# Kernel tuning notes

Measured on AMD Instinct MI355X. Metric: run time of the kernel, lower is better.

The kernel has to match this reference:

```python
import jax, jax.numpy as jnp
import numpy as np

B, S, D = 8, 1024, 1024
H = 16
DK = D // H  # 64, dim_k == dim_v
F = 4096
EPS = 1e-5


def _layernorm(x, w, b):
    mu = jnp.mean(x, axis=-1, keepdims=True)
    var = jnp.mean((x - mu) ** 2, axis=-1, keepdims=True)
    return (x - mu) * jax.lax.rsqrt(var + EPS) * w + b


def setup_inputs() -> dict:
    key = jax.random.key(0)
    ks = jax.random.split(key, 12)
    init = lambda k, shape: (jax.random.normal(k, shape, dtype=jnp.float32) * 0.02)
    return {
        "src": jax.random.normal(ks[0], (B, S, D), dtype=jnp.float32),
        "mask": jnp.zeros((S, S), dtype=jnp.float32),
        # per-head projections, stacked over heads: [H, D, DK]
        "Wq": init(ks[1], (H, D, DK)), "bq": jnp.zeros((H, DK), jnp.float32),
        "Wk": init(ks[2], (H, D, DK)), "bk": jnp.zeros((H, DK), jnp.float32),
        "Wv": init(ks[3], (H, D, DK)), "bv": jnp.zeros((H, DK), jnp.float32),
        "Wo": init(ks[4], (H * DK, D)), "bo": jnp.zeros((D,), jnp.float32),
        "ln1_w": jnp.ones((D,), jnp.float32), "ln1_b": jnp.zeros((D,), jnp.float32),
        "W1": init(ks[5], (D, F)), "b1": jnp.zeros((F,), jnp.float32),
        "W2": init(ks[6], (F, D)), "b2": jnp.zeros((D,), jnp.float32),
        "ln2_w": jnp.ones((D,), jnp.float32), "ln2_b": jnp.zeros((D,), jnp.float32),
    }


def reference(src, mask, Wq, bq, Wk, bk, Wv, bv, Wo, bo,
              ln1_w, ln1_b, W1, b1, W2, b2, ln2_w, ln2_b):
    # per-head projections (vectorized over heads): [B, H, S, DK]
    q = jnp.einsum('bsd,hdk->bhsk', src, Wq) + bq[None, :, None, :]
    k = jnp.einsum('bsd,hdk->bhsk', src, Wk) + bk[None, :, None, :]
    v = jnp.einsum('bsd,hdk->bhsk', src, Wv) + bv[None, :, None, :]
    scale = float(DK) ** 0.5
    logits = jnp.einsum('bhsk,bhtk->bhst', q, k) / scale  # [B,H,S,S]
    logits = logits + mask * (-1e9)
    attn = jax.nn.softmax(logits, axis=-1)
    ctx = jnp.einsum('bhst,bhtv->bhsv', attn, v)  # [B,H,S,DK]
    # concat heads along feature dim (head-major order matches torch cat)
    ctx = jnp.transpose(ctx, (0, 2, 1, 3)).reshape(B, S, H * DK)
    attn_out = ctx @ Wo + bo
    x = _layernorm(src + attn_out, ln1_w, ln1_b)
    ffn = jax.nn.relu(x @ W1 + b1) @ W2 + b2
    return _layernorm(x + ffn, ln2_w, ln2_b)
```

## Files before the change

kernel.cpp:

```cpp
#include <hip/hip_runtime.h>

#define BB 8
#define SS 1024
#define DD 1024
#define HH 16
#define DK 64
#define FF 4096
#define MM (BB*SS)

typedef __attribute__((ext_vector_type(8))) short short8;
typedef __attribute__((ext_vector_type(4))) short short4v;
typedef __attribute__((ext_vector_type(4))) float floatx4;

__device__ inline short f2bf(float f) {
  union { float f; unsigned u; } v; v.f = f;
  unsigned r = (v.u + 0x7FFFu + ((v.u >> 16) & 1u)) >> 16;
  return (short)r;
}
__device__ inline float bf2f(unsigned short u) {
  union { unsigned u; float f; } v; v.u = ((unsigned)u) << 16;
  return v.f;
}

__device__ inline void gload_lds16(const void* g, void* l) {
  __builtin_amdgcn_global_load_lds(
      (const __attribute__((address_space(1))) void*)g,
      (__attribute__((address_space(3))) void*)l, 16, 0, 0);
}

__device__ void tr64(const float* __restrict__ s, unsigned short* __restrict__ d,
                     int R, int C, int r0, int c0, float (*ld)[68], int tid) {
  {
    int r = tid >> 2, c16 = (tid & 3) * 16;
#pragma unroll
    for (int i = 0; i < 4; ++i)
      *(float4*)(&ld[r][c16 + i * 4]) =
          *(const float4*)(s + (size_t)(r0 + r) * C + c0 + c16 + i * 4);
  }
  __syncthreads();
  int c = tid >> 2, r16 = (tid & 3) * 16;
  short8 o0, o1;
#pragma unroll
  for (int i = 0; i < 8; ++i) {
    o0[i] = f2bf(ld[r16 + i][c]);
    o1[i] = f2bf(ld[r16 + 8 + i][c]);
  }
  unsigned short* dp = d + (size_t)(c0 + c) * R + r0 + r16;
  *(short8*)(dp) = o0;
  *(short8*)(dp + 8) = o1;
}

__global__ __launch_bounds__(256) void prep_all(
    const float* __restrict__ src,
    const float* __restrict__ Wq, const float* __restrict__ Wk,
    const float* __restrict__ Wv,
    const float* __restrict__ bq, const float* __restrict__ bk,
    const float* __restrict__ bv, const float* __restrict__ Wo,
    unsigned short* __restrict__ srcb, unsigned short* __restrict__ wqkvT,
    float* __restrict__ bqkv, unsigned short* __restrict__ woT) {
  __shared__ float ld[64][68];
  const int bid = blockIdx.x, tid = threadIdx.x;
  if (bid < 4096) {
    int i8 = (bid * 256 + tid) * 8;
    float4 a = *(const float4*)(src + i8);
    float4 b = *(const float4*)(src + i8 + 4);
    short8 o;
    o[0] = f2bf(a.x); o[1] = f2bf(a.y); o[2] = f2bf(a.z); o[3] = f2bf(a.w);
    o[4] = f2bf(b.x); o[5] = f2bf(b.y); o[6] = f2bf(b.z); o[7] = f2bf(b.w);
    *(short8*)(srcb + i8) = o;
  } else if (bid < 4864) {
    int idx = bid - 4096;
    int d0 = (idx & 15) * 64, h = (idx >> 4) & 15, z = idx >> 8;
    const float* W = (z == 0 ? Wq : z == 1 ? Wk : Wv) + (size_t)h * DD * DK;
    {
      int r = tid >> 2, c16 = (tid & 3) * 16;
#pragma unroll
      for (int i = 0; i < 4; ++i)
        *(float4*)(&ld[r][c16 + i * 4]) =
            *(const float4*)(W + (size_t)(d0 + r) * DK + c16 + i * 4);
    }
    __syncthreads();
    int dv = tid >> 2, d16 = (tid & 3) * 16;
    short8 o0, o1;
#pragma unroll
    for (int i = 0; i < 8; ++i) {
      o0[i] = f2bf(ld[d16 + i][dv]);
      o1[i] = f2bf(ld[d16 + 8 + i][dv]);
    }
    unsigned short* dst = wqkvT + (size_t)(z * 1024 + h * 64 + dv) * DD + d0 + d16;
    *(short8*)(dst) = o0;
    *(short8*)(dst + 8) = o1;
  } else if (bid < 4876) {
    int n = (bid - 4864) * 256 + tid;
    int z = n >> 10;
    const float* s = (z == 0 ? bq : z == 1 ? bk : bv);
    bqkv[n] = s[n & 1023];
  } else {
    int idx = bid - 4876;
    tr64(Wo, woT, 1024, 1024, (idx & 15) * 64, (idx >> 4) * 64, ld, tid);
  }
}

__global__ __launch_bounds__(256) void prep2(
    const unsigned short* __restrict__ qkv, const float* __restrict__ mask,
    const float* __restrict__ W1, const float* __restrict__ W2,
    unsigned short* __restrict__ kbb, unsigned short* __restrict__ vtb,
    unsigned short* __restrict__ maskb, unsigned short* __restrict__ w1T,
    unsigned short* __restrict__ w2T) {
  __shared__ float ldf[64][68];
  const int bid = blockIdx.x, tid = threadIdx.x;
  if (bid < 2048) {
    const int t0 = (bid & 15) * 64, h = (bid >> 4) & 15, b = bid >> 8;
    int row = tid >> 2, c = (tid & 3) * 16;
    const unsigned short* s = qkv + (size_t)(b * SS + t0 + row) * 3072 + 1024 + h * 64 + c;
    unsigned short* d = kbb + ((size_t)((b * HH + h) * SS + t0 + row)) * 64 + c;
    *(short8*)(d) = *(const short8*)(s);
    *(short8*)(d + 8) = *(const short8*)(s + 8);
  } else if (bid < 4096) {
    __shared__ unsigned short ld[64][72];
    const int i = bid - 2048;
    const int t0 = (i & 15) * 64, h = (i >> 4) & 15, b = i >> 8;
    {
      int r = tid >> 2, c16 = (tid & 3) * 16;
      const unsigned short* s = qkv + (size_t)(b * SS + t0 + r) * 3072 + 2048 + h * 64 + c16;
      *(short8*)(&ld[r][c16]) = *(const short8*)(s);
      *(short8*)(&ld[r][c16 + 8]) = *(const short8*)(s + 8);
    }
    __syncthreads();
    int dv = tid >> 2, t16 = (tid & 3) * 16;
    short8 o0, o1;
#pragma unroll
    for (int j = 0; j < 8; ++j) {
      o0[j] = (short)ld[t16 + j][dv];
      o1[j] = (short)ld[t16 + 8 + j][dv];
    }
    unsigned short* d = vtb + ((size_t)(b * HH + h) * DK + dv) * SS + t0 + t16;
    *(short8*)(d) = o0;
    *(short8*)(d + 8) = o1;
  } else if (bid < 4608) {
    int i8 = ((bid - 4096) * 256 + tid) * 8;
    float4 a = *(const float4*)(mask + i8);
    float4 b = *(const float4*)(mask + i8 + 4);
    short8 o;
    o[0] = f2bf(a.x * -1e9f); o[1] = f2bf(a.y * -1e9f);
    o[2] = f2bf(a.z * -1e9f); o[3] = f2bf(a.w * -1e9f);
    o[4] = f2bf(b.x * -1e9f); o[5] = f2bf(b.y * -1e9f);
    o[6] = f2bf(b.z * -1e9f); o[7] = f2bf(b.w * -1e9f);
    *(short8*)(maskb + i8) = o;
  } else if (bid < 5632) {
    int i = bid - 4608;
    tr64(W1, w1T, 1024, 4096, (i & 15) * 64, (i >> 4) * 64, ldf, tid);
  } else {
    int i = bid - 5632;
    tr64(W2, w2T, 4096, 1024, (i & 63) * 64, (i >> 6) * 64, ldf, tid);
  }
}

#define BARE __builtin_amdgcn_s_barrier()
#define VM6  asm volatile("s_waitcnt vmcnt(6)" ::: "memory")
#define VM4  asm volatile("s_waitcnt vmcnt(4)" ::: "memory")
#define VM0  asm volatile("s_waitcnt vmcnt(0)" ::: "memory")
#define PH_HINT asm volatile("s_waitcnt lgkmcnt(8)" ::: "memory")
#define PH_SYNC { \
  __builtin_amdgcn_s_barrier(); \
  asm volatile("s_waitcnt lgkmcnt(0)" ::: "memory"); \
  __builtin_amdgcn_sched_barrier(0); }

#define LOAD_A(lA_, mh_) { \
  _Pragma("unroll") for (int m_ = 0; m_ < 4; ++m_) { \
    const int row_ = wr * 128 + (mh_) * 64 + m_ * 16 + lm; \
    _Pragma("unroll") for (int ks_ = 0; ks_ < 2; ++ks_) \
      a[m_][ks_] = *(const short8*)((lA_) + (size_t)row_ * 64 + \
                     (size_t)(((ks_ * 4 + quad) ^ (lm & 7)) * 8)); \
  } }

#define LOAD_B(lB_, nh_) { \
  _Pragma("unroll") for (int n_ = 0; n_ < 2; ++n_) { \
    const int row_ = wc * 64 + (nh_) * 32 + n_ * 16 + lm; \
    _Pragma("unroll") for (int ks_ = 0; ks_ < 2; ++ks_) \
      bfr[nh_][n_][ks_] = *(const short8*)((lB_) + 16384 + (size_t)row_ * 64 + \
                     (size_t)(((ks_ * 4 + quad) ^ (lm & 7)) * 8)); \
  } }

#define STAGE_A(kt_, mh_, lb_) { \
  _Pragma("unroll") for (int c_ = 0; c_ < 2; ++c_) { \
    const int row_ = c_ * 128 + (mh_) * 64; \
    gload_lds16(gA + (size_t)(kt_) * 64 + (size_t)row_ * K, \
                (lb_) + (size_t)(row_ + wave * 8) * 64); \
  } }

#define STAGE_B(kt_, nh_, lb_) { \
  _Pragma("unroll") for (int c_ = 0; c_ < 2; ++c_) { \
    const int row_ = c_ * 128 + hi128 + (nh_) * 32; \
    gload_lds16(gB + (size_t)(kt_) * 64 + (size_t)row_ * K, \
                (lb_) + 16384 + (size_t)(row_ + (wave & 3) * 8) * 64); \
  } }

#define MFMA_PH(mh_, nh_) { \
  __builtin_amdgcn_s_setprio(1); \
  _Pragma("unroll") for (int m_ = 0; m_ < 4; ++m_) \
    _Pragma("unroll") for (int n_ = 0; n_ < 2; ++n_) { \
      acc[(mh_) * 4 + m_][(nh_) * 2 + n_] = __builtin_amdgcn_mfma_f32_16x16x32_bf16( \
          bfr[nh_][n_][0], a[m_][0], acc[(mh_) * 4 + m_][(nh_) * 2 + n_], 0, 0, 0); \
      acc[(mh_) * 4 + m_][(nh_) * 2 + n_] = __builtin_amdgcn_mfma_f32_16x16x32_bf16( \
          bfr[nh_][n_][1], a[m_][1], acc[(mh_) * 4 + m_][(nh_) * 2 + n_], 0, 0, 0); \
    } \
  __builtin_amdgcn_s_setprio(0); }

#define KITER(e_, ST_) { \
  LOAD_A(buf0, 0); LOAD_B(buf0, 0); \
  STAGE_B((e_) + 1, 1, buf1); \
  PH_HINT; PH_SYNC; MFMA_PH(0, 0); BARE; \
  LOAD_B(buf0, 1); \
  if (ST_) STAGE_A((e_) + 2, 0, buf0); \
  PH_SYNC; MFMA_PH(0, 1); BARE; \
  LOAD_A(buf0, 1); \
  if (ST_) STAGE_B((e_) + 2, 0, buf0); \
  PH_SYNC; MFMA_PH(1, 0); BARE; \
  if (ST_) STAGE_A((e_) + 2, 1, buf0); \
  PH_SYNC; MFMA_PH(1, 1); \
  if (ST_) { VM6; } else { VM0; } \
  BARE; \
  LOAD_A(buf1, 0); LOAD_B(buf1, 0); \
  if (ST_) STAGE_B((e_) + 2, 1, buf0); \
  PH_HINT; PH_SYNC; MFMA_PH(0, 0); BARE; \
  LOAD_B(buf1, 1); \
  if (ST_) STAGE_A((e_) + 3, 0, buf1); \
  PH_SYNC; MFMA_PH(0, 1); BARE; \
  LOAD_A(buf1, 1); \
  if (ST_) STAGE_B((e_) + 3, 0, buf1); \
  PH_SYNC; MFMA_PH(1, 0); BARE; \
  if (ST_) { \
    STAGE_A((e_) + 3, 1, buf1); \
    PH_SYNC; MFMA_PH(1, 1); VM6; BARE; \
  } else { \
    PH_SYNC; MFMA_PH(1, 1); \
  } }

template <int RELU>
__global__ __launch_bounds__(512, 2) void gemm256(
    const unsigned short* __restrict__ A, const unsigned short* __restrict__ Bt,
    const float* __restrict__ bias, unsigned short* __restrict__ C,
    int M, int N, int K) {
  extern __shared__ unsigned short lds[];
  unsigned short* buf0 = lds;
  unsigned short* buf1 = lds + 32768;
  const int tid = threadIdx.x;
  const int wave = tid >> 6, lane = tid & 63;
  const int lm = lane & 15, quad = lane >> 4;
  const int wr = wave >> 2, wc = wave & 3;

  const int nwg = gridDim.x;
  const int cpx = nwg >> 3;
  const int id = (blockIdx.x & 7) * cpx + (blockIdx.x >> 3);
  const int nbx = N >> 8;
  const int bx = id % nbx, by = id / nbx;
  const int n0 = bx << 8, m0 = by << 8;

  const int NT = K >> 6;

  const int srow = tid >> 3;
  const int chs = (tid & 7) ^ (srow & 7);
  const int hi128 = (tid >= 256) ? 64 : 0;
  const int r32 = (tid >> 3) & 31;
  const unsigned short* gA = A + (size_t)(m0 + srow) * K + chs * 8;
  const unsigned short* gB = Bt + (size_t)(n0 + r32) * K + chs * 8;

  floatx4 acc[8][4] = {};
  short8 a[4][2], bfr[2][2][2];

  STAGE_A(0, 0, buf0); STAGE_B(0, 0, buf0);
  STAGE_A(0, 1, buf0); STAGE_B(0, 1, buf0);
  STAGE_A(1, 0, buf1); STAGE_B(1, 0, buf1);
  STAGE_A(1, 1, buf1);
  VM6;
  BARE;

  const int TT = NT >> 1;
  for (int i = 0; i < TT - 1; ++i) {
    KITER(2 * i, 1);
  }
  KITER(NT - 2, 0);

#pragma unroll
  for (int mi = 0; mi < 8; ++mi) {
    const int row = m0 + wr * 128 + mi * 16 + lm;
#pragma unroll
    for (int nj = 0; nj < 4; ++nj) {
      const int col = n0 + wc * 64 + nj * 16 + (quad << 2);
      const float4 bv = *(const float4*)(bias + col);
      float vv[4] = {acc[mi][nj][0] + bv.x, acc[mi][nj][1] + bv.y,
                     acc[mi][nj][2] + bv.z, acc[mi][nj][3] + bv.w};
      short4v o;
#pragma unroll
      for (int r = 0; r < 4; ++r) {
        float v = vv[r];
        if (RELU) v = fmaxf(v, 0.f);
        o[r] = f2bf(v);
      }
      *(short4v*)(C + (size_t)row * N + col) = o;
    }
  }
}

#define LOAD_A1(lb_, mh_) { \
  _Pragma("unroll") for (int m_ = 0; m_ < 2; ++m_) { \
    const int row_ = wr * 64 + (mh_) * 32 + m_ * 16 + lm; \
    _Pragma("unroll") for (int ks_ = 0; ks_ < 2; ++ks_) \
      a[m_][ks_] = *(const short8*)((lb_) + (size_t)row_ * 64 + \
                     (size_t)(((ks_ * 4 + quad) ^ (lm & 7)) * 8)); \
  } }

#define LOAD_B1(lb_, nh_) { \
  _Pragma("unroll") for (int n_ = 0; n_ < 2; ++n_) { \
    const int row_ = wc * 64 + (nh_) * 32 + n_ * 16 + lm; \
    _Pragma("unroll") for (int ks_ = 0; ks_ < 2; ++ks_) \
      bfr[nh_][n_][ks_] = *(const short8*)((lb_) + 8192 + (size_t)row_ * 64 + \
                     (size_t)(((ks_ * 4 + quad) ^ (lm & 7)) * 8)); \
  } }

#define STAGE_A1(kt_, mh_, lb_) { \
  gload_lds16(gA + (size_t)(kt_) * 64 + (size_t)((mh_) * 32) * K, \
              (lb_) + (size_t)((mh_) * 32 + hi128 + (wave & 3) * 8) * 64); }

#define STAGE_B1(kt_, nh_, lb_) { \
  _Pragma("unroll") for (int c_ = 0; c_ < 2; ++c_) { \
    const int row_ = c_ * 128 + hi128 + (nh_) * 32; \
    gload_lds16(gB + (size_t)(kt_) * 64 + (size_t)row_ * K, \
                (lb_) + 8192 + (size_t)(row_ + (wave & 3) * 8) * 64); \
  } }

#define MFMA_PH1(mh_, nh_) { \
  __builtin_amdgcn_s_setprio(1); \
  _Pragma("unroll") for (int m_ = 0; m_ < 2; ++m_) \
    _Pragma("unroll") for (int n_ = 0; n_ < 2; ++n_) { \
      acc[(mh_) * 2 + m_][(nh_) * 2 + n_] = __builtin_amdgcn_mfma_f32_16x16x32_bf16( \
          bfr[nh_][n_][0], a[m_][0], acc[(mh_) * 2 + m_][(nh_) * 2 + n_], 0, 0, 0); \
      acc[(mh_) * 2 + m_][(nh_) * 2 + n_] = __builtin_amdgcn_mfma_f32_16x16x32_bf16( \
          bfr[nh_][n_][1], a[m_][1], acc[(mh_) * 2 + m_][(nh_) * 2 + n_], 0, 0, 0); \
    } \
  __builtin_amdgcn_s_setprio(0); }

#define KITER1(e_, ST_) { \
  LOAD_A1(buf0, 0); LOAD_B1(buf0, 0); \
  STAGE_B1((e_) + 1, 1, buf1); \
  PH_SYNC; MFMA_PH1(0, 0); BARE; \
  LOAD_B1(buf0, 1); \
  if (ST_) STAGE_A1((e_) + 2, 0, buf0); \
  PH_SYNC; MFMA_PH1(0, 1); BARE; \
  LOAD_A1(buf0, 1); \
  if (ST_) STAGE_B1((e_) + 2, 0, buf0); \
  PH_SYNC; MFMA_PH1(1, 0); BARE; \
  if (ST_) STAGE_A1((e_) + 2, 1, buf0); \
  PH_SYNC; MFMA_PH1(1, 1); \
  if (ST_) { VM4; } else { VM0; } \
  BARE; \
  LOAD_A1(buf1, 0); LOAD_B1(buf1, 0); \
  if (ST_) STAGE_B1((e_) + 2, 1, buf0); \
  PH_SYNC; MFMA_PH1(0, 0); BARE; \
  LOAD_B1(buf1, 1); \
  if (ST_) STAGE_A1((e_) + 3, 0, buf1); \
  PH_SYNC; MFMA_PH1(0, 1); BARE; \
  LOAD_A1(buf1, 1); \
  if (ST_) STAGE_B1((e_) + 3, 0, buf1); \
  PH_SYNC; MFMA_PH1(1, 0); BARE; \
  if (ST_) { \
    STAGE_A1((e_) + 3, 1, buf1); \
    PH_SYNC; MFMA_PH1(1, 1); VM4; BARE; \
  } else { \
    PH_SYNC; MFMA_PH1(1, 1); \
  } }

__global__ __launch_bounds__(512, 2) void gemm128(
    const unsigned short* __restrict__ A, const unsigned short* __restrict__ Bt,
    const float* __restrict__ bias, unsigned short* __restrict__ C,
    int M, int N, int K) {
  extern __shared__ unsigned short lds[];
  unsigned short* buf0 = lds;
  unsigned short* buf1 = lds + 24576;
  const int tid = threadIdx.x;
  const int wave = tid >> 6, lane = tid & 63;
  const int lm = lane & 15, quad = lane >> 4;
  const int wr = wave >> 2, wc = wave & 3;

  const int nwg = gridDim.x;
  const int cpx = nwg >> 3;
  const int id = (blockIdx.x & 7) * cpx + (blockIdx.x >> 3);
  const int nbx = N >> 8;
  const int bx = id % nbx, by = id / nbx;
  const int n0 = bx << 8, m0 = by << 7;

  const int NT = K >> 6;

  const int srow = tid >> 3;
  const int chs = (tid & 7) ^ (srow & 7);
  const int hi128 = (tid >= 256) ? 64 : 0;
  const int r32 = (tid >> 3) & 31;
  const unsigned short* gA = A + (size_t)(m0 + hi128 + r32) * K + chs * 8;
  const unsigned short* gB = Bt + (size_t)(n0 + r32) * K + chs * 8;

  floatx4 acc[4][4] = {};
  short8 a[2][2], bfr[2][2][2];

  STAGE_A1(0, 0, buf0); STAGE_B1(0, 0, buf0);
  STAGE_A1(0, 1, buf0); STAGE_B1(0, 1, buf0);
  STAGE_A1(1, 0, buf1); STAGE_B1(1, 0, buf1);
  STAGE_A1(1, 1, buf1);
  VM4;
  BARE;

  const int TT = NT >> 1;
  for (int i = 0; i < TT - 1; ++i) {
    KITER1(2 * i, 1);
  }
  KITER1(NT - 2, 0);

#pragma unroll
  for (int mi = 0; mi < 4; ++mi) {
    const int row = m0 + wr * 64 + mi * 16 + lm;
#pragma unroll
    for (int nj = 0; nj < 4; ++nj) {
      const int col = n0 + wc * 64 + nj * 16 + (quad << 2);
      const float4 bv = *(const float4*)(bias + col);
      short4v o;
      o[0] = f2bf(acc[mi][nj][0] + bv.x);
      o[1] = f2bf(acc[mi][nj][1] + bv.y);
      o[2] = f2bf(acc[mi][nj][2] + bv.z);
      o[3] = f2bf(acc[mi][nj][3] + bv.w);
      *(short4v*)(C + (size_t)row * N + col) = o;
    }
  }
}

__global__ __launch_bounds__(512) void attention_flash(
    const unsigned short* __restrict__ qkv, const unsigned short* __restrict__ kb,
    const unsigned short* __restrict__ vt, const unsigned short* __restrict__ maskb,
    unsigned short* __restrict__ ctx) {
  const int flat = blockIdx.x;
  const int bh = (flat & 7) + 8 * (flat >> 6);
  const int qt = (flat >> 3) & 7;
  const int b = bh >> 4, h = bh & 15;
  const int s0 = qt * 128;
  const int tid = threadIdx.x;
  const int wave = tid >> 6, lane = tid & 63;
  const int lm = lane & 15, quad = lane >> 4;

  __shared__ __align__(16) unsigned short Ks[64 * 64];
  __shared__ __align__(16) unsigned short Vs[64 * 64];
  __shared__ __align__(16) unsigned short Ms[128 * 64];
  __shared__ __align__(16) unsigned short Ps[8][16 * 72];

  const unsigned short* qp = qkv + (size_t)(b * SS + s0 + wave * 16 + lm) * 3072 + h * 64;
  const short8 qa0 = *(const short8*)(qp + quad * 8);
  const short8 qa1 = *(const short8*)(qp + quad * 8 + 32);

  const unsigned short* kbase = kb + (size_t)bh * SS * DK;
  const unsigned short* vbase = vt + (size_t)bh * DK * SS;
  const unsigned short* mbase = maskb + (size_t)s0 * SS;

  const int sr = lane >> 3, sj = lane & 7;
  float m_run = -3e38f, l_run = 0.f;
  floatx4 O[4] = {};

  for (int it = 0; it < 16; ++it) {
    const int t0 = it * 64;
    __syncthreads();
    {
      int r = wave * 8 + sr;
      gload_lds16(kbase + (size_t)(t0 + r) * 64 + (size_t)(sj ^ (r & 7)) * 8,
                  (char*)Ks + wave * 1024);
      gload_lds16(vbase + (size_t)r * SS + t0 + (size_t)(sj ^ (r & 7)) * 8,
                  (char*)Vs + wave * 1024);
      int q1 = wave * 8 + sr;
      gload_lds16(mbase + (size_t)q1 * SS + t0 + (size_t)(sj ^ (q1 & 7)) * 8,
                  (char*)Ms + wave * 1024);
      int q2 = 64 + wave * 8 + sr;
      gload_lds16(mbase + (size_t)q2 * SS + t0 + (size_t)(sj ^ (q2 & 7)) * 8,
                  (char*)Ms + 8192 + wave * 1024);
    }
    __syncthreads();

    float p[16];
    float mt = -3e38f;
    const int qr = wave * 16 + lm;
#pragma unroll
    for (int ts = 0; ts < 4; ++ts) {
      int r = ts * 16 + lm;
      short8 kf0 = *(const short8*)&Ks[(r * 8 + (quad ^ (r & 7))) * 8];
      short8 kf1 = *(const short8*)&Ks[(r * 8 + ((quad + 4) ^ (r & 7))) * 8];
      floatx4 c = {0.f, 0.f, 0.f, 0.f};
      c = __builtin_amdgcn_mfma_f32_16x16x32_bf16(kf0, qa0, c, 0, 0, 0);
      c = __builtin_amdgcn_mfma_f32_16x16x32_bf16(kf1, qa1, c, 0, 0, 0);
      int mj = (ts * 2 + (quad >> 1)) ^ (qr & 7);
      short4v mv = *(const short4v*)&Ms[(qr * 8 + mj) * 8 + (quad & 1) * 4];
#pragma unroll
      for (int r2 = 0; r2 < 4; ++r2) {
        float sv = c[r2] * 0.125f + bf2f((unsigned short)mv[r2]);
        p[ts * 4 + r2] = sv;
        mt = fmaxf(mt, sv);
      }
    }
    mt = fmaxf(mt, __shfl_xor(mt, 16));
    mt = fmaxf(mt, __shfl_xor(mt, 32));
    if (!__all(mt - m_run <= 8.f)) {
      float mnew = fmaxf(m_run, mt);
      float alpha = __expf(m_run - mnew);
#pragma unroll
      for (int d = 0; d < 4; ++d)
#pragma unroll
        for (int r2 = 0; r2 < 4; ++r2) O[d][r2] *= alpha;
      l_run *= alpha;
      m_run = mnew;
    }
    float psum = 0.f;
#pragma unroll
    for (int i = 0; i < 16; ++i) { p[i] = __expf(p[i] - m_run); psum += p[i]; }
    psum += __shfl_xor(psum, 16);
    psum += __shfl_xor(psum, 32);
    l_run += psum;

    unsigned short* pw = &Ps[wave][lm * 72];
#pragma unroll
    for (int ts = 0; ts < 4; ++ts) {
      unsigned plo, phi;
      asm("v_cvt_pk_bf16_f32 %0, %1, %2" : "=v"(plo) : "v"(p[ts * 4 + 0]), "v"(p[ts * 4 + 1]));
      asm("v_cvt_pk_bf16_f32 %0, %1, %2" : "=v"(phi) : "v"(p[ts * 4 + 2]), "v"(p[ts * 4 + 3]));
      uint2 pu; pu.x = plo; pu.y = phi;
      *(uint2*)(pw + ts * 16 + quad * 4) = pu;
    }

#pragma unroll
    for (int ks = 0; ks < 2; ++ks) {
      short8 pf = *(const short8*)(pw + ks * 32 + quad * 8);
#pragma unroll
      for (int d = 0; d < 4; ++d) {
        int dv = d * 16 + lm;
        short8 vf = *(const short8*)&Vs[(dv * 8 + ((ks * 4 + quad) ^ (dv & 7))) * 8];
        O[d] = __builtin_amdgcn_mfma_f32_16x16x32_bf16(vf, pf, O[d], 0, 0, 0);
      }
    }
  }

  const float inv = 1.f / l_run;
  unsigned short* cp = ctx + (size_t)(b * SS + s0 + wave * 16 + lm) * DD + h * 64;
#pragma unroll
  for (int d = 0; d < 4; ++d) {
    short4v o;
#pragma unroll
    for (int r2 = 0; r2 < 4; ++r2) o[r2] = f2bf(O[d][r2] * inv);
    *(short4v*)(cp + d * 16 + quad * 4) = o;
  }
}

template <int A_BF16, int OUT_BF16>
__global__ __launch_bounds__(256) void residual_ln(
    const void* __restrict__ a_, const unsigned short* __restrict__ rr,
    const float* __restrict__ w, const float* __restrict__ bias,
    void* __restrict__ out_) {
  const int row = blockIdx.x;
  const int t = threadIdx.x;
  float x[4];
  if (A_BF16) {
    short4v va = *(const short4v*)((const unsigned short*)a_ + (size_t)row * DD + t * 4);
#pragma unroll
    for (int i = 0; i < 4; ++i) x[i] = bf2f((unsigned short)va[i]);
  } else {
    float4 va = *(const float4*)((const float*)a_ + (size_t)row * DD + t * 4);
    x[0] = va.x; x[1] = va.y; x[2] = va.z; x[3] = va.w;
  }
  {
    short4v vr = *(const short4v*)(rr + (size_t)row * DD + t * 4);
#pragma unroll
    for (int i = 0; i < 4; ++i) x[i] += bf2f((unsigned short)vr[i]);
  }
  float s = 0.f, ss = 0.f;
#pragma unroll
  for (int i = 0; i < 4; ++i) { s += x[i]; ss += x[i] * x[i]; }
#pragma unroll
  for (int o = 32; o > 0; o >>= 1) {
    s  += __shfl_down(s, o);
    ss += __shfl_down(ss, o);
  }
  __shared__ float2 sred[4];
  int wid = t >> 6;
  if ((t & 63) == 0) sred[wid] = make_float2(s, ss);
  __syncthreads();
  float st = 0.f, sst = 0.f;
#pragma unroll
  for (int i = 0; i < 4; ++i) { st += sred[i].x; sst += sred[i].y; }
  float mu  = st * (1.f / 1024.f);
  float var = sst * (1.f / 1024.f) - mu * mu;
  float rsq = rsqrtf(var + 1e-5f);
  float4 vw = *(const float4*)(w + t * 4);
  float4 vb = *(const float4*)(bias + t * 4);
  float o[4];
  o[0] = (x[0] - mu) * rsq * vw.x + vb.x;
  o[1] = (x[1] - mu) * rsq * vw.y + vb.y;
  o[2] = (x[2] - mu) * rsq * vw.z + vb.z;
  o[3] = (x[3] - mu) * rsq * vw.w + vb.w;
  if (OUT_BF16) {
    short4v ov;
#pragma unroll
    for (int i = 0; i < 4; ++i) ov[i] = f2bf(o[i]);
    *(short4v*)((unsigned short*)out_ + (size_t)row * DD + t * 4) = ov;
  } else {
    float4 ov = {o[0], o[1], o[2], o[3]};
    *(float4*)((float*)out_ + (size_t)row * DD + t * 4) = ov;
  }
}

extern "C" void kernel_launch(void* const* d_in, const int* in_sizes, int n_in,
                              void* d_out, int out_size, void* d_ws, size_t ws_size,
                              hipStream_t stream) {
  const float* src  = (const float*)d_in[0];
  const float* mask = (const float*)d_in[1];
  const float* Wq = (const float*)d_in[2];  const float* bq = (const float*)d_in[3];
  const float* Wk = (const float*)d_in[4];  const float* bk = (const float*)d_in[5];
  const float* Wv = (const float*)d_in[6];  const float* bv = (const float*)d_in[7];
  const float* Wo = (const float*)d_in[8];  const float* bo = (const float*)d_in[9];
  const float* ln1w = (const float*)d_in[10]; const float* ln1b = (const float*)d_in[11];
  const float* W1 = (const float*)d_in[12]; const float* b1 = (const float*)d_in[13];
  const float* W2 = (const float*)d_in[14]; const float* b2 = (const float*)d_in[15];
  const float* ln2w = (const float*)d_in[16]; const float* ln2b = (const float*)d_in[17];
  float* out = (float*)d_out;

  const size_t NEED = 125841408;
  if (ws_size < NEED) return;

  char* ws = (char*)d_ws;
  unsigned short* qkv   = (unsigned short*)(ws);
  unsigned short* vtb   = (unsigned short*)(ws + 50331648);
  unsigned short* kbb   = (unsigned short*)(ws + 67108864);
  unsigned short* ctxb  = (unsigned short*)(ws + 83886080);
  unsigned short* srcb  = (unsigned short*)(ws + 100663296);
  unsigned short* w1T   = (unsigned short*)(ws + 100663296);
  unsigned short* w2T   = (unsigned short*)(ws + 109051904);
  unsigned short* wqkvT = (unsigned short*)(ws + 117440512);
  unsigned short* maskb = (unsigned short*)(ws + 117440512);
  unsigned short* woT   = (unsigned short*)(ws + 123731968);
  float*          bqkv  = (float*)(ws + 125829120);
  unsigned short* h1       = qkv;
  unsigned short* attn_out = kbb;
  unsigned short* xb       = ctxb;
  unsigned short* ffn      = kbb;

  static bool lds_init = false;
  if (!lds_init) {
    auto* k0 = gemm256<0>;
    auto* k1 = gemm256<1>;
    hipFuncSetAttribute((const void*)k0, hipFuncAttributeMaxDynamicSharedMemorySize, 131072);
    hipFuncSetAttribute((const void*)k1, hipFuncAttributeMaxDynamicSharedMemorySize, 131072);
    hipFuncSetAttribute((const void*)gemm128, hipFuncAttributeMaxDynamicSharedMemorySize, 98304);
    lds_init = true;
  }

  prep_all<<<5132, 256, 0, stream>>>(src, Wq, Wk, Wv, bq, bk, bv, Wo,
                                     srcb, wqkvT, bqkv, woT);
  gemm128<<<(3072 / 256) * (MM / 128), 512, 98304, stream>>>(srcb, wqkvT, bqkv, qkv, MM, 3072, DD);
  prep2<<<6656, 256, 0, stream>>>(qkv, mask, W1, W2, kbb, vtb, maskb, w1T, w2T);
  attention_flash<<<1024, 512, 0, stream>>>(qkv, kbb, vtb, maskb, ctxb);
  gemm128<<<(DD / 256) * (MM / 128), 512, 98304, stream>>>(ctxb, woT, bo, attn_out, MM, DD, DD);
  residual_ln<0, 1><<<MM, 256, 0, stream>>>(src, attn_out, ln1w, ln1b, xb);
  gemm256<1><<<(FF / 256) * (MM / 256), 512, 131072, stream>>>(xb, w1T, b1, h1, MM, FF, DD);
  gemm128<<<(DD / 256) * (MM / 128), 512, 98304, stream>>>(h1, w2T, b2, ffn, MM, DD, FF);
  residual_ln<1, 0><<<MM, 256, 0, stream>>>(xb, ffn, ln2w, ln2b, out);
}
```

Baseline: 509.8 us.

## Use exp2 softmax with prescaled logits and persistent two-tile FFN1 GEMM

The attention softmax now folds log2(e) into the QK scale and the mask constant, so exp2 replaces expf. The rescale threshold is adjusted to match, and the row max is computed with a balanced fmax tree. The FFN1 GEMM launches half the workgroups, and each one computes two M tiles in sequence with a barrier between them, which cuts the number of waves and the tail effect. The attention K-load address is also hoisted out of the loop. Looping over two tiles keeps the same LDS usage but serialises two tiles per block, which could lower latency hiding.

```diff
diff --git a/kernel.cpp b/kernel.cpp
--- a/kernel.cpp
+++ b/kernel.cpp
@@ -138,14 +138,15 @@
     *(short8*)(d) = o0;
     *(short8*)(d + 8) = o1;
   } else if (bid < 4608) {
+    const float MS = -1.442695041e9f;
     int i8 = ((bid - 4096) * 256 + tid) * 8;
     float4 a = *(const float4*)(mask + i8);
     float4 b = *(const float4*)(mask + i8 + 4);
     short8 o;
-    o[0] = f2bf(a.x * -1e9f); o[1] = f2bf(a.y * -1e9f);
-    o[2] = f2bf(a.z * -1e9f); o[3] = f2bf(a.w * -1e9f);
-    o[4] = f2bf(b.x * -1e9f); o[5] = f2bf(b.y * -1e9f);
-    o[6] = f2bf(b.z * -1e9f); o[7] = f2bf(b.w * -1e9f);
+    o[0] = f2bf(a.x * MS); o[1] = f2bf(a.y * MS);
+    o[2] = f2bf(a.z * MS); o[3] = f2bf(a.w * MS);
+    o[4] = f2bf(b.x * MS); o[5] = f2bf(b.y * MS);
+    o[6] = f2bf(b.z * MS); o[7] = f2bf(b.w * MS);
     *(short8*)(maskb + i8) = o;
   } else if (bid < 5632) {
     int i = bid - 4608;
@@ -237,7 +238,7 @@
     PH_SYNC; MFMA_PH(1, 1); \
   } }
 
-template <int RELU>
+template <int RELU, int REPS>
 __global__ __launch_bounds__(512, 2) void gemm256(
     const unsigned short* __restrict__ A, const unsigned short* __restrict__ Bt,
     const float* __restrict__ bias, unsigned short* __restrict__ C,
@@ -254,8 +255,9 @@
   const int cpx = nwg >> 3;
   const int id = (blockIdx.x & 7) * cpx + (blockIdx.x >> 3);
   const int nbx = N >> 8;
-  const int bx = id % nbx, by = id / nbx;
-  const int n0 = bx << 8, m0 = by << 8;
+  const int bx = id % nbx, by0 = id / nbx;
+  const int n0 = bx << 8;
+  const int bystep = (M >> 8) / REPS;
 
   const int NT = K >> 6;
 
@@ -263,43 +265,48 @@
   const int chs = (tid & 7) ^ (srow & 7);
   const int hi128 = (tid >= 256) ? 64 : 0;
   const int r32 = (tid >> 3) & 31;
-  const unsigned short* gA = A + (size_t)(m0 + srow) * K + chs * 8;
   const unsigned short* gB = Bt + (size_t)(n0 + r32) * K + chs * 8;
 
-  floatx4 acc[8][4] = {};
-  short8 a[4][2], bfr[2][2][2];
-
-  STAGE_A(0, 0, buf0); STAGE_B(0, 0, buf0);
-  STAGE_A(0, 1, buf0); STAGE_B(0, 1, buf0);
-  STAGE_A(1, 0, buf1); STAGE_B(1, 0, buf1);
-  STAGE_A(1, 1, buf1);
-  VM6;
-  BARE;
-
-  const int TT = NT >> 1;
-  for (int i = 0; i < TT - 1; ++i) {
-    KITER(2 * i, 1);
-  }
-  KITER(NT - 2, 0);
-
-#pragma unroll
-  for (int mi = 0; mi < 8; ++mi) {
-    const int row = m0 + wr * 128 + mi * 16 + lm;
-#pragma unroll
-    for (int nj = 0; nj < 4; ++nj) {
-      const int col = n0 + wc * 64 + nj * 16 + (quad << 2);
-      const float4 bv = *(const float4*)(bias + col);
-      float vv[4] = {acc[mi][nj][0] + bv.x, acc[mi][nj][1] + bv.y,
-                     acc[mi][nj][2] + bv.z, acc[mi][nj][3] + bv.w};
-      short4v o;
-#pragma unroll
-      for (int r = 0; r < 4; ++r) {
-        float v = vv[r];
-        if (RELU) v = fmaxf(v, 0.f);
-        o[r] = f2bf(v);
+  for (int rep = 0; rep < REPS; ++rep) {
+    const int m0 = (by0 + rep * bystep) << 8;
+    const unsigned short* gA = A + (size_t)(m0 + srow) * K + chs * 8;
+
+    floatx4 acc[8][4] = {};
+    short8 a[4][2], bfr[2][2][2];
+
+    STAGE_A(0, 0, buf0); STAGE_B(0, 0, buf0);
+    STAGE_A(0, 1, buf0); STAGE_B(0, 1, buf0);
+    STAGE_A(1, 0, buf1); STAGE_B(1, 0, buf1);
+    STAGE_A(1, 1, buf1);
+    VM6;
+    BARE;
+
+    const int TT = NT >> 1;
+    for (int i = 0; i < TT - 1; ++i) {
+      KITER(2 * i, 1);
+    }
+    KITER(NT - 2, 0);
+
+#pragma unroll
+    for (int mi = 0; mi < 8; ++mi) {
+      const int row = m0 + wr * 128 + mi * 16 + lm;
+#pragma unroll
+      for (int nj = 0; nj < 4; ++nj) {
+        const int col = n0 + wc * 64 + nj * 16 + (quad << 2);
+        const float4 bv = *(const float4*)(bias + col);
+        float vv[4] = {acc[mi][nj][0] + bv.x, acc[mi][nj][1] + bv.y,
+                       acc[mi][nj][2] + bv.z, acc[mi][nj][3] + bv.w};
+        short4v o;
+#pragma unroll
+        for (int r = 0; r < 4; ++r) {
+          float v = vv[r];
+          if (RELU) v = fmaxf(v, 0.f);
+          o[r] = f2bf(v);
+        }
+        *(short4v*)(C + (size_t)row * N + col) = o;
       }
-      *(short4v*)(C + (size_t)row * N + col) = o;
-    }
+    }
+    if (rep + 1 < REPS) { BARE; }
   }
 }
 
@@ -459,6 +466,8 @@
   const unsigned short* mbase = maskb + (size_t)s0 * SS;
 
   const int sr = lane >> 3, sj = lane & 7;
+  const int srr = wave * 8 + sr;
+  const unsigned short* ksrc = kbase + (size_t)srr * 64 + (size_t)(sj ^ (srr & 7)) * 8;
   float m_run = -3e38f, l_run = 0.f;
   floatx4 O[4] = {};
 
@@ -466,10 +475,8 @@
     const int t0 = it * 64;
     __syncthreads();
     {
-      int r = wave * 8 + sr;
-      gload_lds16(kbase + (size_t)(t0 + r) * 64 + (size_t)(sj ^ (r & 7)) * 8,
-                  (char*)Ks + wave * 1024);
-      gload_lds16(vbase + (size_t)r * SS + t0 + (size_t)(sj ^ (r & 7)) * 8,
+      gload_lds16(ksrc + (size_t)t0 * 64, (char*)Ks + wave * 1024);
+      gload_lds16(vbase + (size_t)srr * SS + t0 + (size_t)(sj ^ (srr & 7)) * 8,
                   (char*)Vs + wave * 1024);
       int q1 = wave * 8 + sr;
       gload_lds16(mbase + (size_t)q1 * SS + t0 + (size_t)(sj ^ (q1 & 7)) * 8,
@@ -481,7 +488,6 @@
     __syncthreads();
 
     float p[16];
-    float mt = -3e38f;
     const int qr = wave * 16 + lm;
 #pragma unroll
     for (int ts = 0; ts < 4; ++ts) {
@@ -495,16 +501,20 @@
       short4v mv = *(const short4v*)&Ms[(qr * 8 + mj) * 8 + (quad & 1) * 4];
 #pragma unroll
       for (int r2 = 0; r2 < 4; ++r2) {
-        float sv = c[r2] * 0.125f + bf2f((unsigned short)mv[r2]);
-        p[ts * 4 + r2] = sv;
-        mt = fmaxf(mt, sv);
+        p[ts * 4 + r2] = c[r2] * 0.18033688011112042f + bf2f((unsigned short)mv[r2]);
       }
     }
+    float m0a = fmaxf(fmaxf(p[0], p[1]), p[2]);
+    float m0b = fmaxf(fmaxf(p[3], p[4]), p[5]);
+    float m0c = fmaxf(fmaxf(p[6], p[7]), p[8]);
+    float m0d = fmaxf(fmaxf(p[9], p[10]), p[11]);
+    float m0e = fmaxf(fmaxf(p[12], p[13]), p[14]);
+    float mt = fmaxf(fmaxf(fmaxf(m0a, m0b), m0c), fmaxf(fmaxf(m0d, m0e), p[15]));
     mt = fmaxf(mt, __shfl_xor(mt, 16));
     mt = fmaxf(mt, __shfl_xor(mt, 32));
-    if (!__all(mt - m_run <= 8.f)) {
+    if (!__all(mt - m_run <= 11.541560327f)) {
       float mnew = fmaxf(m_run, mt);
-      float alpha = __expf(m_run - mnew);
+      float alpha = __builtin_amdgcn_exp2f(m_run - mnew);
 #pragma unroll
       for (int d = 0; d < 4; ++d)
 #pragma unroll
@@ -514,7 +524,10 @@
     }
     float psum = 0.f;
 #pragma unroll
-    for (int i = 0; i < 16; ++i) { p[i] = __expf(p[i] - m_run); psum += p[i]; }
+    for (int i = 0; i < 16; ++i) {
+      p[i] = __builtin_amdgcn_exp2f(p[i] - m_run);
+      psum += p[i];
+    }
     psum += __shfl_xor(psum, 16);
     psum += __shfl_xor(psum, 32);
     l_run += psum;
@@ -646,9 +659,7 @@
 
   static bool lds_init = false;
   if (!lds_init) {
-    auto* k0 = gemm256<0>;
-    auto* k1 = gemm256<1>;
-    hipFuncSetAttribute((const void*)k0, hipFuncAttributeMaxDynamicSharedMemorySize, 131072);
+    auto* k1 = gemm256<1, 2>;
     hipFuncSetAttribute((const void*)k1, hipFuncAttributeMaxDynamicSharedMemorySize, 131072);
     hipFuncSetAttribute((const void*)gemm128, hipFuncAttributeMaxDynamicSharedMemorySize, 98304);
     lds_init = true;
@@ -661,7 +672,7 @@
   attention_flash<<<1024, 512, 0, stream>>>(qkv, kbb, vtb, maskb, ctxb);
   gemm128<<<(DD / 256) * (MM / 128), 512, 98304, stream>>>(ctxb, woT, bo, attn_out, MM, DD, DD);
   residual_ln<0, 1><<<MM, 256, 0, stream>>>(src, attn_out, ln1w, ln1b, xb);
-  gemm256<1><<<(FF / 256) * (MM / 256), 512, 131072, stream>>>(xb, w1T, b1, h1, MM, FF, DD);
+  gemm256<1, 2><<<(FF / 256) * (MM / 256) / 2, 512, 131072, stream>>>(xb, w1T, b1, h1, MM, FF, DD);
   gemm128<<<(DD / 256) * (MM / 128), 512, 98304, stream>>>(h1, w2T, b2, ffn, MM, DD, FF);
   residual_ln<1, 0><<<MM, 256, 0, stream>>>(xb, ffn, ln2w, ln2b, out);
 }
```

Measured after the change: 485.2 us. -4.8%, faster.
